# Kernel tuning notes

Hardware: AMD Instinct MI355X
Metric: run time of the kernel (lower is better)

The kernel has to match this reference:

```python
import jax, jax.numpy as jnp
import numpy as np

BATCH = 2048      # rays
NINTRS = 256      # samples per ray (intersections has NINTRS+1 t-values)
VALID = 128       # valid samples per ray (mask pattern: first VALID of each ray)
NUM_ATOMS = 256   # grid.data_dim: dictionary size
SH_DIM = 9        # (sh_deg+1)^2, sh_deg=2
DATA_DIM = 3 * SH_DIM + 1  # 28: rgb SH coeffs + sigma
RESOLUTION = 256.0
WHITE_BKGD = True


def sh_basis_deg2(dirs):
    # dirs: (B, 3) -> (B, 9) real SH basis up to degree 2
    d = dirs / jnp.linalg.norm(dirs, axis=-1, keepdims=True)
    x, y, z = d[:, 0], d[:, 1], d[:, 2]
    one = jnp.ones_like(x)
    return jnp.stack([
        0.28209479177387814 * one,
        -0.4886025119029199 * y,
        0.4886025119029199 * z,
        -0.4886025119029199 * x,
        1.0925484305920792 * x * y,
        -1.0925484305920792 * y * z,
        0.31539156525252005 * (2.0 * z * z - x * x - y * y),
        -1.0925484305920792 * x * z,
        0.5462742152960396 * (x * x - y * y),
    ], axis=-1)


def setup_inputs() -> dict:
    key = jax.random.key(0)
    k1, k2, k3, k4, k5 = jax.random.split(key, 5)
    n_pts = BATCH * VALID
    queries = jax.random.normal(k1, (n_pts, NUM_ATOMS), dtype=jnp.float32) * 0.05
    atoms = jax.random.normal(k2, (NUM_ATOMS, DATA_DIM, 8), dtype=jnp.float32) * 0.1
    intrs_pts = jax.random.uniform(k3, (n_pts, 3), minval=-1.0, maxval=1.0, dtype=jnp.float32)
    deltas = jax.random.uniform(k4, (BATCH, NINTRS + 1), minval=0.01, maxval=0.05, dtype=jnp.float32)
    intersections = 2.0 + jnp.cumsum(deltas, axis=-1)  # sorted t-values per ray
    rays_d = jax.random.normal(k5, (BATCH, 3), dtype=jnp.float32)
    rays_d = rays_d / jnp.linalg.norm(rays_d, axis=-1, keepdims=True)
    # mask pattern: first VALID samples of each ray -> flat row-major indices
    b = np.arange(BATCH)[:, None]
    i = np.arange(VALID)[None, :]
    flat_idx = jnp.asarray((b * NINTRS + i).reshape(-1), dtype=jnp.int32)
    return {"queries": queries, "atoms": atoms, "intrs_pts": intrs_pts,
            "intersections": intersections, "rays_d": rays_d, "flat_idx": flat_idx}


def reference(queries, atoms, intrs_pts, intersections, rays_d, flat_idx):
    n_pts = queries.shape[0]
    # sparse-dictionary decode: (n_pts, num_atoms) @ (num_atoms, data_dim*8)
    data_masked = (queries @ atoms.reshape(NUM_ATOMS, -1)).reshape(n_pts, DATA_DIM, 8)

    # trilinear interpolation over the 8 corners (xyzs computed under no_grad)
    pts = jax.lax.stop_gradient(intrs_pts * (RESOLUTION / 2.0) + 1e-05)
    xyzs = pts - jnp.floor(pts)
    x, y, z = xyzs[:, 0], xyzs[:, 1], xyzs[:, 2]
    cx = jnp.stack([1.0 - x, x], axis=-1)  # (n, 2)
    cy = jnp.stack([1.0 - y, y], axis=-1)
    cz = jnp.stack([1.0 - z, z], axis=-1)
    w = (cx[:, :, None, None] * cy[:, None, :, None] * cz[:, None, None, :]).reshape(n_pts, 8)
    data_interp = jnp.einsum('ndc,nc->nd', data_masked, w)  # (n_pts, data_dim)

    # scatter sigma into ray-indexed buffer (masked_scatter_ equivalent)
    sigma_masked = data_interp[:, -1]
    sigma = jnp.zeros((BATCH * NINTRS,), dtype=sigma_masked.dtype).at[flat_idx].set(sigma_masked)
    sigma = jax.nn.relu(sigma.reshape(BATCH, NINTRS))

    # sigma2alpha: alpha compositing weights
    dists = (intersections[:, 1:] - intersections[:, :-1]) * jnp.linalg.norm(rays_d, axis=-1, keepdims=True)
    alpha = 1.0 - jnp.exp(-sigma * dists)
    trans = jnp.cumprod(1.0 - alpha + 1e-10, axis=-1)
    trans = jnp.concatenate([jnp.ones((BATCH, 1), dtype=alpha.dtype), trans[:, :-1]], axis=-1)
    abs_light = alpha * trans  # (batch, nintrs)

    # SH color reconstruction per masked point
    sh_mult_full = sh_basis_deg2(rays_d)                 # (batch, sh_dim)
    ray_idx = flat_idx // NINTRS
    sh_mult = sh_mult_full[ray_idx]                      # (n_pts, sh_dim)
    sh_masked = data_interp[:, :-1].reshape(n_pts, 3, SH_DIM)
    rgb_masked = jnp.sum(sh_mult[:, None, :] * sh_masked, axis=-1)  # (n_pts, 3)
    rgb = jnp.zeros((BATCH * NINTRS, 3), dtype=rgb_masked.dtype).at[flat_idx].set(rgb_masked)
    rgb = rgb.reshape(BATCH, NINTRS, 3)

    # shrgb2rgb: sigmoid + composite (+ white background)
    rgb = jax.nn.sigmoid(rgb)
    rgb = jnp.sum(abs_light[:, :, None] * rgb, axis=1)
    if WHITE_BKGD:
        rgb = rgb + (1.0 - jnp.sum(abs_light, axis=-1, keepdims=True))

    # depth_map: expected t at interval midpoints
    mids = 0.5 * (intersections[:, 1:] + intersections[:, :-1])
    depth = jnp.sum(abs_light * mids, axis=-1)
    return rgb, alpha, depth
```

## Files before the change

kernel.cpp:

```cpp
#include <hip/hip_runtime.h>
#include <hip/hip_bf16.h>
#include <math.h>

#define BATCH   2048
#define NINTRS  256
#define VALID   128
#define NATOMS  256
#define DDIM    28

typedef float  f32x4  __attribute__((ext_vector_type(4)));
typedef short  bf16x8 __attribute__((ext_vector_type(8)));

__device__ __forceinline__ unsigned short f32_to_bf16(float f) {
    unsigned int u = __float_as_uint(f);
    u = (u + 0x7FFFu + ((u >> 16) & 1u)) >> 16;
    return (unsigned short)u;
}

__global__ __launch_bounds__(256)
void build_atomsB(const float* __restrict__ atoms, unsigned short* __restrict__ ab)
{
    const int t = blockIdx.x * 256 + threadIdx.x;
    const int d = t >> 8;
    const int a = t & 255;
    const float* src = atoms + ((size_t)a * DDIM + d) * 8;
    f32x4 v0 = *(const f32x4*)(src);
    f32x4 v1 = *(const f32x4*)(src + 4);
    bf16x8 o;
    #pragma unroll
    for (int j = 0; j < 4; ++j) {
        o[j]   = (short)f32_to_bf16(v0[j]);
        o[j+4] = (short)f32_to_bf16(v1[j]);
    }
    *(bf16x8*)(ab + (size_t)t * 8) = o;
}

__global__ __launch_bounds__(256, 2)
void shdict_fused(const float* __restrict__ q,
                  const unsigned short* __restrict__ ab,
                  const float* __restrict__ ipts,
                  const float* __restrict__ intr,
                  const float* __restrict__ raysd,
                  float* __restrict__ out_rgb,
                  float* __restrict__ out_alpha,
                  float* __restrict__ out_depth)
{
    __shared__ char  bs[32 * 256 * 2];
    __shared__ float qbuf[3 * 4 * 1024];
    __shared__ float w_lds[VALID][9];
    __shared__ float pr_lds[VALID][5];

    const int ray  = blockIdx.x;
    const int tid  = threadIdx.x;
    const int lane = tid & 63;
    const int wav  = tid >> 6;

    const float rdx = raysd[ray*3+0], rdy = raysd[ray*3+1], rdz = raysd[ray*3+2];
    float px = 0.f, py = 0.f, pz = 0.f;
    if (tid < VALID) {
        const int n = ray * VALID + tid;
        px = ipts[n*3+0]*128.0f + 1e-5f;
        py = ipts[n*3+1]*128.0f + 1e-5f;
        pz = ipts[n*3+2]*128.0f + 1e-5f;
    }
    asm volatile("s_waitcnt vmcnt(0)" ::: "memory");

    bf16x8 abv[28];
    #pragma unroll
    for (int d = 0; d < 28; ++d)
        abv[d] = *(const bf16x8*)(ab + ((size_t)(d * 256 + tid)) * 8);

    const int srow   = lane >> 3;
    const int schunk = (lane & 7) ^ srow;
    const char* gq = (const char*)q
        + ((size_t)(ray * VALID + wav * 32 + srow) << 10)
        + ((size_t)schunk << 4);
    char* lq = (char*)qbuf + (wav << 12);

    auto stage_q = [&](int ks, int bufi) {
        #pragma unroll
        for (int j = 0; j < 4; ++j) {
            __builtin_amdgcn_global_load_lds(
                (const __attribute__((address_space(1))) void*)(gq + ks * 128 + j * 8192),
                (__attribute__((address_space(3))) void*)(lq + bufi * 16384 + j * 1024),
                16, 0, 0);
        }
    };

    stage_q(0, 0);
    stage_q(1, 1);
    stage_q(2, 2);

    const float ss = rdx*rdx + rdy*rdy + rdz*rdz;
    const float rn = rsqrtf(ss);
    const float x = rdx*rn, y = rdy*rn, z = rdz*rn;
    float sh[9];
    sh[0] = 0.28209479177387814f;
    sh[1] = -0.4886025119029199f * y;
    sh[2] =  0.4886025119029199f * z;
    sh[3] = -0.4886025119029199f * x;
    sh[4] =  1.0925484305920792f * x * y;
    sh[5] = -1.0925484305920792f * y * z;
    sh[6] =  0.31539156525252005f * (2.0f*z*z - x*x - y*y);
    sh[7] = -1.0925484305920792f * x * z;
    sh[8] =  0.5462742152960396f * (x*x - y*y);

    {
        const int a = tid;
        float accB[3][8];
        #pragma unroll
        for (int k = 0; k < 3; ++k)
            #pragma unroll
            for (int c = 0; c < 8; ++c) accB[k][c] = 0.0f;
        #pragma unroll
        for (int d = 0; d < 27; ++d) {
            const int kp = d / 9, j = d - kp * 9;
            const float s = sh[j];
            const unsigned int* u = (const unsigned int*)&abv[d];
            #pragma unroll
            for (int i = 0; i < 4; ++i) {
                const float flo = __uint_as_float(u[i] << 16);
                const float fhi = __uint_as_float(u[i] & 0xffff0000u);
                accB[kp][2*i]   = fmaf(s, flo, accB[kp][2*i]);
                accB[kp][2*i+1] = fmaf(s, fhi, accB[kp][2*i+1]);
            }
        }
        #pragma unroll
        for (int kp = 0; kp < 3; ++kp)
            #pragma unroll
            for (int c = 0; c < 8; ++c) {
                const int col = kp*8 + c;
                unsigned byte = ((unsigned)col << 9) + ((unsigned)a << 1);
                byte ^= (unsigned)((col & 7) << 4);
                *(unsigned short*)(bs + byte) = f32_to_bf16(accB[kp][c]);
            }
        const unsigned short* sv = (const unsigned short*)&abv[27];
        #pragma unroll
        for (int c = 0; c < 8; ++c) {
            const int col = 24 + c;
            unsigned byte = ((unsigned)col << 9) + ((unsigned)a << 1);
            byte ^= (unsigned)((col & 7) << 4);
            *(unsigned short*)(bs + byte) = sv[c];
        }
    }

    if (tid < VALID) {
        const float fx = px - floorf(px);
        const float fy = py - floorf(py);
        const float fz = pz - floorf(pz);
        #pragma unroll
        for (int c = 0; c < 8; ++c) {
            const float wx = (c & 4) ? fx : 1.0f - fx;
            const float wy = (c & 2) ? fy : 1.0f - fy;
            const float wz = (c & 1) ? fz : 1.0f - fz;
            w_lds[tid][c] = wx * wy * wz;
        }
    }
    __syncthreads();

    f32x4 acc[2][2];
    #pragma unroll
    for (int m = 0; m < 2; ++m)
        #pragma unroll
        for (int n = 0; n < 2; ++n)
            acc[m][n] = (f32x4){0.f, 0.f, 0.f, 0.f};

    const int row  = lane & 15;
    const int kgrp = lane >> 4;
    const int key  = row & 7;

    #pragma unroll
    for (int ks = 0; ks < 8; ++ks) {
        if (ks < 6)      asm volatile("s_waitcnt vmcnt(8)" ::: "memory");
        else if (ks == 6) asm volatile("s_waitcnt vmcnt(4)" ::: "memory");
        else              asm volatile("s_waitcnt vmcnt(0)" ::: "memory");

        const char* rb = (char*)qbuf + (ks % 3) * 16384 + (wav << 12);
        f32x4 a0l = *(const f32x4*)(rb + row*128      + (((2*kgrp+0) ^ key) << 4));
        f32x4 a0h = *(const f32x4*)(rb + row*128      + (((2*kgrp+1) ^ key) << 4));
        f32x4 a1l = *(const f32x4*)(rb + (row+16)*128 + (((2*kgrp+0) ^ key) << 4));
        f32x4 a1h = *(const f32x4*)(rb + (row+16)*128 + (((2*kgrp+1) ^ key) << 4));
        bf16x8 af0, af1;
        #pragma unroll
        for (int j = 0; j < 4; ++j) {
            af0[j]   = (short)f32_to_bf16(a0l[j]);
            af0[j+4] = (short)f32_to_bf16(a0h[j]);
            af1[j]   = (short)f32_to_bf16(a1l[j]);
            af1[j+4] = (short)f32_to_bf16(a1h[j]);
        }

        bf16x8 bfrag[2];
        const int abase = ks*32 + kgrp*8;
        #pragma unroll
        for (int nt = 0; nt < 2; ++nt) {
            const int col = nt*16 + row;
            unsigned byte = ((unsigned)col << 9) + ((unsigned)abase << 1);
            byte ^= (unsigned)((col & 7) << 4);
            bfrag[nt] = *(const bf16x8*)(bs + byte);
        }

        asm volatile("s_waitcnt lgkmcnt(0)" ::: "memory");
        if (ks + 3 < 8) stage_q(ks + 3, ks % 3);

        acc[0][0] = __builtin_amdgcn_mfma_f32_16x16x32_bf16(af0, bfrag[0], acc[0][0], 0, 0, 0);
        acc[0][1] = __builtin_amdgcn_mfma_f32_16x16x32_bf16(af0, bfrag[1], acc[0][1], 0, 0, 0);
        acc[1][0] = __builtin_amdgcn_mfma_f32_16x16x32_bf16(af1, bfrag[0], acc[1][0], 0, 0, 0);
        acc[1][1] = __builtin_amdgcn_mfma_f32_16x16x32_bf16(af1, bfrag[1], acc[1][1], 0, 0, 0);
    }

    const int cc  = lane & 7;
    const int kph = (lane & 15) >> 3;
    #pragma unroll
    for (int m = 0; m < 2; ++m) {
        const int ptb = wav*32 + m*16 + kgrp*4;
        #pragma unroll
        for (int nt = 0; nt < 2; ++nt) {
            const int kp = nt*2 + kph;
            #pragma unroll
            for (int r = 0; r < 4; ++r) {
                float t = acc[m][nt][r] * w_lds[ptb + r][cc];
                t += __shfl_xor(t, 1);
                t += __shfl_xor(t, 2);
                t += __shfl_xor(t, 4);
                if (cc == 0) pr_lds[ptb + r][kp] = t;
            }
        }
    }
    __syncthreads();

    if (wav == 0) {
        const float rnorm = sqrtf(ss);
        const int i0 = lane * 2;
        const float t0 = intr[ray*257 + i0];
        const float t1 = intr[ray*257 + i0 + 1];
        const float t2 = intr[ray*257 + i0 + 2];
        const float d0 = (t1 - t0) * rnorm;
        const float d1 = (t2 - t1) * rnorm;
        const float s0 = fmaxf(pr_lds[i0][3],     0.0f);
        const float s1 = fmaxf(pr_lds[i0 + 1][3], 0.0f);
        const float a0 = 1.0f - __expf(-s0 * d0);
        const float a1 = 1.0f - __expf(-s1 * d1);
        const float f0 = 1.0f - a0 + 1e-10f;
        const float f1 = 1.0f - a1 + 1e-10f;

        float pprod = f0 * f1;
        #pragma unroll
        for (int off = 1; off < 64; off <<= 1) {
            float v = __shfl_up(pprod, off);
            if (lane >= off) pprod *= v;
        }
        float excl = __shfl_up(pprod, 1);
        if (lane == 0) excl = 1.0f;

        const float tr0 = excl;
        const float tr1 = excl * f0;
        const float al0 = a0 * tr0;
        const float al1 = a1 * tr1;
        const float mid0 = 0.5f * (t0 + t1);
        const float mid1 = 0.5f * (t1 + t2);

        const float r0 = 1.0f / (1.0f + __expf(-pr_lds[i0][0]));
        const float g0 = 1.0f / (1.0f + __expf(-pr_lds[i0][1]));
        const float b0 = 1.0f / (1.0f + __expf(-pr_lds[i0][2]));
        const float r1 = 1.0f / (1.0f + __expf(-pr_lds[i0 + 1][0]));
        const float g1 = 1.0f / (1.0f + __expf(-pr_lds[i0 + 1][1]));
        const float b1 = 1.0f / (1.0f + __expf(-pr_lds[i0 + 1][2]));

        float sum_r = al0*r0 + al1*r1;
        float sum_g = al0*g0 + al1*g1;
        float sum_b = al0*b0 + al1*b1;
        float sum_d = al0*mid0 + al1*mid1;
        float sum_a = al0 + al1;
        #pragma unroll
        for (int off = 1; off < 64; off <<= 1) {
            sum_r += __shfl_xor(sum_r, off);
            sum_g += __shfl_xor(sum_g, off);
            sum_b += __shfl_xor(sum_b, off);
            sum_d += __shfl_xor(sum_d, off);
            sum_a += __shfl_xor(sum_a, off);
        }
        if (lane == 0) {
            const float bkgd = 1.0f - sum_a;
            out_rgb[ray*3 + 0] = sum_r + bkgd;
            out_rgb[ray*3 + 1] = sum_g + bkgd;
            out_rgb[ray*3 + 2] = sum_b + bkgd;
            out_depth[ray]     = sum_d;
        }
        float2 av; av.x = a0; av.y = a1;
        *(float2*)(out_alpha + (size_t)ray*NINTRS + i0) = av;
        float2 zz; zz.x = 0.0f; zz.y = 0.0f;
        *(float2*)(out_alpha + (size_t)ray*NINTRS + VALID + i0) = zz;
    }
}

extern "C" void kernel_launch(void* const* d_in, const int* in_sizes, int n_in,
                              void* d_out, int out_size, void* d_ws, size_t ws_size,
                              hipStream_t stream)
{
    const float* q     = (const float*)d_in[0];
    const float* atoms = (const float*)d_in[1];
    const float* ipts  = (const float*)d_in[2];
    const float* intr  = (const float*)d_in[3];
    const float* raysd = (const float*)d_in[4];

    float* out = (float*)d_out;
    float* out_rgb   = out;
    float* out_alpha = out + BATCH*3;
    float* out_depth = out + BATCH*3 + (size_t)BATCH*NINTRS;

    unsigned short* ab = (unsigned short*)d_ws;

    build_atomsB<<<28, 256, 0, stream>>>(atoms, ab);
    shdict_fused<<<BATCH, 256, 0, stream>>>(q, ab, ipts, intr, raysd,
                                            out_rgb, out_alpha, out_depth);
}
```

Baseline: 62.75 us.

## Load query tiles directly into registers instead of staging through LDS

Removes the 48KB LDS triple buffer for query rows and instead prefetches each wave's A-fragments straight into registers with inline-asm global loads, three k-steps ahead. This drops the LDS round trip and frees shared memory, so the launch bound is raised to three blocks per SM to increase occupancy. It risks register pressure from 48 extra prefetch VGPRs plus the 28 bf16x8 atom vectors held per thread, and uncoalesced row-strided global reads. The inline-asm waitcnt bookkeeping must stay consistent with the compiler's other outstanding loads.

Measured after the change: 58.81 us. 6.3% less time.

```diff
diff --git a/kernel.cpp b/kernel.cpp
--- a/kernel.cpp
+++ b/kernel.cpp
@@ -35,7 +35,7 @@
     *(bf16x8*)(ab + (size_t)t * 8) = o;
 }
 
-__global__ __launch_bounds__(256, 2)
+__global__ __launch_bounds__(256, 3)
 void shdict_fused(const float* __restrict__ q,
                   const unsigned short* __restrict__ ab,
                   const float* __restrict__ ipts,
@@ -46,7 +46,6 @@
                   float* __restrict__ out_depth)
 {
     __shared__ char  bs[32 * 256 * 2];
-    __shared__ float qbuf[3 * 4 * 1024];
     __shared__ float w_lds[VALID][9];
     __shared__ float pr_lds[VALID][5];
 
@@ -63,33 +62,11 @@
         py = ipts[n*3+1]*128.0f + 1e-5f;
         pz = ipts[n*3+2]*128.0f + 1e-5f;
     }
-    asm volatile("s_waitcnt vmcnt(0)" ::: "memory");
 
     bf16x8 abv[28];
     #pragma unroll
     for (int d = 0; d < 28; ++d)
         abv[d] = *(const bf16x8*)(ab + ((size_t)(d * 256 + tid)) * 8);
-
-    const int srow   = lane >> 3;
-    const int schunk = (lane & 7) ^ srow;
-    const char* gq = (const char*)q
-        + ((size_t)(ray * VALID + wav * 32 + srow) << 10)
-        + ((size_t)schunk << 4);
-    char* lq = (char*)qbuf + (wav << 12);
-
-    auto stage_q = [&](int ks, int bufi) {
-        #pragma unroll
-        for (int j = 0; j < 4; ++j) {
-            __builtin_amdgcn_global_load_lds(
-                (const __attribute__((address_space(1))) void*)(gq + ks * 128 + j * 8192),
-                (__attribute__((address_space(3))) void*)(lq + bufi * 16384 + j * 1024),
-                16, 0, 0);
-        }
-    };
-
-    stage_q(0, 0);
-    stage_q(1, 1);
-    stage_q(2, 2);
 
     const float ss = rdx*rdx + rdy*rdy + rdz*rdz;
     const float rn = rsqrtf(ss);
@@ -156,7 +133,30 @@
             w_lds[tid][c] = wx * wy * wz;
         }
     }
-    __syncthreads();
+
+    const int row  = lane & 15;
+    const int kgrp = lane >> 4;
+    const float* ga0 = q + (size_t)(ray*VALID + wav*32 + row) * NATOMS + kgrp*8;
+    const float* ga1 = ga0 + 16 * NATOMS;
+
+    f32x4 pf[3][4];
+
+#define ISSUE_STEP(s, kk) do {                                                   \
+    const float* _p0 = ga0 + (kk)*32;                                            \
+    const float* _p1 = ga1 + (kk)*32;                                            \
+    asm volatile("global_load_dwordx4 %0, %1, off" : "=v"(pf[s][0]) : "v"(_p0)   : "memory"); \
+    asm volatile("global_load_dwordx4 %0, %1, off" : "=v"(pf[s][1]) : "v"(_p0+4) : "memory"); \
+    asm volatile("global_load_dwordx4 %0, %1, off" : "=v"(pf[s][2]) : "v"(_p1)   : "memory"); \
+    asm volatile("global_load_dwordx4 %0, %1, off" : "=v"(pf[s][3]) : "v"(_p1+4) : "memory"); \
+} while (0)
+
+    asm volatile("s_waitcnt vmcnt(0)" ::: "memory");
+    ISSUE_STEP(0, 0);
+    ISSUE_STEP(1, 1);
+    ISSUE_STEP(2, 2);
+
+    asm volatile("s_waitcnt lgkmcnt(0)" ::: "memory");
+    __builtin_amdgcn_s_barrier();
 
     f32x4 acc[2][2];
     #pragma unroll
@@ -165,29 +165,24 @@
         for (int n = 0; n < 2; ++n)
             acc[m][n] = (f32x4){0.f, 0.f, 0.f, 0.f};
 
-    const int row  = lane & 15;
-    const int kgrp = lane >> 4;
-    const int key  = row & 7;
-
     #pragma unroll
     for (int ks = 0; ks < 8; ++ks) {
-        if (ks < 6)      asm volatile("s_waitcnt vmcnt(8)" ::: "memory");
+        if (ks <= 5)      asm volatile("s_waitcnt vmcnt(8)" ::: "memory");
         else if (ks == 6) asm volatile("s_waitcnt vmcnt(4)" ::: "memory");
         else              asm volatile("s_waitcnt vmcnt(0)" ::: "memory");
-
-        const char* rb = (char*)qbuf + (ks % 3) * 16384 + (wav << 12);
-        f32x4 a0l = *(const f32x4*)(rb + row*128      + (((2*kgrp+0) ^ key) << 4));
-        f32x4 a0h = *(const f32x4*)(rb + row*128      + (((2*kgrp+1) ^ key) << 4));
-        f32x4 a1l = *(const f32x4*)(rb + (row+16)*128 + (((2*kgrp+0) ^ key) << 4));
-        f32x4 a1h = *(const f32x4*)(rb + (row+16)*128 + (((2*kgrp+1) ^ key) << 4));
+        __builtin_amdgcn_sched_barrier(0);
+
+        const int s = ks % 3;
         bf16x8 af0, af1;
         #pragma unroll
         for (int j = 0; j < 4; ++j) {
-            af0[j]   = (short)f32_to_bf16(a0l[j]);
-            af0[j+4] = (short)f32_to_bf16(a0h[j]);
-            af1[j]   = (short)f32_to_bf16(a1l[j]);
-            af1[j+4] = (short)f32_to_bf16(a1h[j]);
-        }
+            af0[j]   = (short)f32_to_bf16(pf[s][0][j]);
+            af0[j+4] = (short)f32_to_bf16(pf[s][1][j]);
+            af1[j]   = (short)f32_to_bf16(pf[s][2][j]);
+            af1[j+4] = (short)f32_to_bf16(pf[s][3][j]);
+        }
+
+        if (ks + 3 < 8) ISSUE_STEP(s, ks + 3);
 
         bf16x8 bfrag[2];
         const int abase = ks*32 + kgrp*8;
@@ -199,14 +194,12 @@
             bfrag[nt] = *(const bf16x8*)(bs + byte);
         }
 
-        asm volatile("s_waitcnt lgkmcnt(0)" ::: "memory");
-        if (ks + 3 < 8) stage_q(ks + 3, ks % 3);
-
         acc[0][0] = __builtin_amdgcn_mfma_f32_16x16x32_bf16(af0, bfrag[0], acc[0][0], 0, 0, 0);
         acc[0][1] = __builtin_amdgcn_mfma_f32_16x16x32_bf16(af0, bfrag[1], acc[0][1], 0, 0, 0);
         acc[1][0] = __builtin_amdgcn_mfma_f32_16x16x32_bf16(af1, bfrag[0], acc[1][0], 0, 0, 0);
         acc[1][1] = __builtin_amdgcn_mfma_f32_16x16x32_bf16(af1, bfrag[1], acc[1][1], 0, 0, 0);
     }
+#undef ISSUE_STEP
 
     const int cc  = lane & 7;
     const int kph = (lane & 15) >> 3;
```
